# Kernel tuning notes

Measured on AMD Instinct MI355X. Metric: run time of the kernel, lower is better.

## Reference

```python
import jax, jax.numpy as jnp
import numpy as np

N_HEADS = 16
D_EMBED = 1024
HEAD_DIM = D_EMBED // N_HEADS


def setup_inputs() -> dict:
    key = jax.random.key(0)
    ks = jax.random.split(key, 9)
    s = 1.0 / np.sqrt(D_EMBED)
    def lin(kw, kb):
        W = jax.random.uniform(kw, (D_EMBED, D_EMBED), jnp.float32, -s, s)
        b = jax.random.uniform(kb, (D_EMBED,), jnp.float32, -s, s)
        return W, b
    q_w, q_b = lin(ks[0], ks[1])
    k_w, k_b = lin(ks[2], ks[3])
    v_w, v_b = lin(ks[4], ks[5])
    o_w, o_b = lin(ks[6], ks[7])
    x = jax.random.normal(ks[8], (4, 2048, D_EMBED), jnp.float32)
    return {"x": x, "q_w": q_w, "q_b": q_b, "k_w": k_w, "k_b": k_b,
            "v_w": v_w, "v_b": v_b, "o_w": o_w, "o_b": o_b}


def reference(x, q_w, q_b, k_w, k_b, v_w, v_b, o_w, o_b):
    B, S, _ = x.shape
    # projections; W stored as [in, out] so y = x @ W + b (matches nn.Linear math)
    def split_heads(y):
        return y.reshape(B, S, N_HEADS, HEAD_DIM).transpose(0, 2, 1, 3)  # [B,H,S,D]
    q = split_heads(x @ q_w + q_b)
    k = split_heads(x @ k_w + k_b)
    v = split_heads(x @ v_w + v_b)
    scale = 1.0 / np.sqrt(HEAD_DIM).astype(np.float32)
    scores = jnp.einsum('bhqd,bhkd->bhqk', q, k) * scale  # [B,H,S,S]
    weights = jax.nn.softmax(scores, axis=-1)
    attn = jnp.einsum('bhqk,bhkd->bhqd', weights, v)  # [B,H,S,D]
    attn = attn.transpose(0, 2, 1, 3).reshape(B, S, D_EMBED)
    return attn @ o_w + o_b
```

## Files before the change

### kernel.cpp

```cpp
#include <hip/hip_runtime.h>
#include <hip/hip_bf16.h>
#include <math.h>

typedef __attribute__((ext_vector_type(8))) short bf16x8;
typedef __attribute__((ext_vector_type(4))) float f32x4;

#define D_EMBED 1024
#define SEQ 2048
#define NH 16
#define HD 64
#define QSCALE 0.1803368801111204f

__device__ __forceinline__ short f2bf(float f) {
    union { float f; unsigned u; } v; v.f = f;
    return (short)((v.u + 0x7FFFu + ((v.u >> 16) & 1u)) >> 16);
}

__device__ __forceinline__ unsigned pk_bf16(float a, float b) {
#if __has_builtin(__builtin_amdgcn_cvt_pk_bf16_f32)
    typedef __attribute__((ext_vector_type(2))) __bf16 vbf2;
    union { vbf2 v; unsigned u; } c;
    c.v = __builtin_amdgcn_cvt_pk_bf16_f32(a, b);
    return c.u;
#else
    return (unsigned)(unsigned short)f2bf(a) | ((unsigned)(unsigned short)f2bf(b) << 16);
#endif
}

__device__ __forceinline__ float exp2f_(float x) {
#if __has_builtin(__builtin_amdgcn_exp2f)
    return __builtin_amdgcn_exp2f(x);
#else
    return __expf(x * 0.6931471805599453f);
#endif
}

typedef __attribute__((address_space(1))) const void gvoid_t;
typedef __attribute__((address_space(3))) void lvoid_t;
__device__ __forceinline__ void glds16(const void* g, void* l) {
    __builtin_amdgcn_global_load_lds((gvoid_t*)g, (lvoid_t*)l, 16, 0, 0);
}

__global__ __launch_bounds__(256) void xconv_kernel(const float* __restrict__ x,
                                                    short* __restrict__ xb)
{
    size_t i = ((size_t)blockIdx.x * 256 + threadIdx.x) * 8;
    float4 f0 = *(const float4*)(x + i);
    float4 f1 = *(const float4*)(x + i + 4);
    uint4 o;
    o.x = pk_bf16(f0.x, f0.y); o.y = pk_bf16(f0.z, f0.w);
    o.z = pk_bf16(f1.x, f1.y); o.w = pk_bf16(f1.z, f1.w);
    *(uint4*)(xb + i) = o;
}

__global__ __launch_bounds__(256) void wtrans_kernel(
    const float* __restrict__ w0, const float* __restrict__ w1,
    const float* __restrict__ w2, const float* __restrict__ w3,
    short* __restrict__ wt)
{
    __shared__ float tile[64][65];
    const float* W = (blockIdx.z == 0) ? w0 : (blockIdx.z == 1) ? w1
                   : (blockIdx.z == 2) ? w2 : w3;
    short* out = wt + (size_t)blockIdx.z * D_EMBED * D_EMBED;
    int k0 = blockIdx.x * 64, n0 = blockIdx.y * 64;
    #pragma unroll
    for (int i = 0; i < 16; i++) {
        int idx = threadIdx.x + i * 256; int r = idx >> 6, c = idx & 63;
        tile[r][c] = W[(size_t)(k0 + r) * D_EMBED + n0 + c];
    }
    __syncthreads();
    #pragma unroll
    for (int i = 0; i < 16; i++) {
        int idx = threadIdx.x + i * 256; int r = idx >> 6, c = idx & 63;
        out[(size_t)(n0 + r) * D_EMBED + k0 + c] = f2bf(tile[c][r]);
    }
}

__global__ __launch_bounds__(256) void gemm_qkv_kernel(
    const short* __restrict__ xb, const short* __restrict__ wt,
    const float* __restrict__ qb, const float* __restrict__ kb, const float* __restrict__ vb,
    short* __restrict__ qo, short* __restrict__ ko, short* __restrict__ vto)
{
    __shared__ __attribute__((aligned(16))) short As[128][32];
    __shared__ __attribute__((aligned(16))) short Bs[128][32];
    const int tid = threadIdx.x;
    const int lane = tid & 63, wv = tid >> 6;
    const int l16 = lane & 15, quad = lane >> 4;
    const int wm = (wv & 1) * 64, wn = (wv >> 1) * 64;
    const int m0 = blockIdx.y * 128, n0 = blockIdx.x * 128;

    const short* aptr0 = xb + (size_t)(m0 + (tid >> 2)) * D_EMBED + (tid & 3) * 8;
    const short* aptr1 = aptr0 + (size_t)64 * D_EMBED;
    const short* bptr0 = wt + (size_t)(n0 + (tid >> 2)) * D_EMBED + (tid & 3) * 8;
    const short* bptr1 = bptr0 + (size_t)64 * D_EMBED;
    char* aldsb = (char*)&As[0][0] + wv * 1024;
    char* bldsb = (char*)&Bs[0][0] + wv * 1024;

    f32x4 acc[4][4];
    #pragma unroll
    for (int a = 0; a < 4; a++)
        #pragma unroll
        for (int b = 0; b < 4; b++) acc[a][b] = (f32x4){0.f, 0.f, 0.f, 0.f};

    for (int k0 = 0; k0 < D_EMBED; k0 += 32) {
        __syncthreads();
        glds16(aptr0 + k0, aldsb);
        glds16(aptr1 + k0, aldsb + 4096);
        glds16(bptr0 + k0, bldsb);
        glds16(bptr1 + k0, bldsb + 4096);
        __syncthreads();
        bf16x8 af[4], bfr[4];
        #pragma unroll
        for (int mi = 0; mi < 4; mi++) af[mi]  = *(const bf16x8*)&As[wm + mi * 16 + l16][quad * 8];
        #pragma unroll
        for (int ni = 0; ni < 4; ni++) bfr[ni] = *(const bf16x8*)&Bs[wn + ni * 16 + l16][quad * 8];
        #pragma unroll
        for (int mi = 0; mi < 4; mi++)
            #pragma unroll
            for (int ni = 0; ni < 4; ni++)
                acc[mi][ni] = __builtin_amdgcn_mfma_f32_16x16x32_bf16(af[mi], bfr[ni], acc[mi][ni], 0, 0, 0);
    }

    const int zz = n0 >> 10;
    const int ncol0 = (n0 & 1023) + wn;
    const float* bias = (zz == 0) ? qb : (zz == 1) ? kb : vb;
    #pragma unroll
    for (int mi = 0; mi < 4; mi++)
        #pragma unroll
        for (int ni = 0; ni < 4; ni++)
            #pragma unroll
            for (int rg = 0; rg < 4; rg++) {
                int row = m0 + wm + mi * 16 + quad * 4 + rg;
                int col = ncol0 + ni * 16 + l16;
                float v = acc[mi][ni][rg] + bias[col];
                int b = row >> 11, s = row & 2047, h = col >> 6, d = col & 63;
                if (zz == 0)      qo[(((size_t)(b * NH + h)) * SEQ + s) * HD + d] = f2bf(v * QSCALE);
                else if (zz == 1) ko[(((size_t)(b * NH + h)) * SEQ + s) * HD + d] = f2bf(v);
                else              vto[(((size_t)(b * NH + h)) * HD + d) * SEQ + s] = f2bf(v);
            }
}

__global__ __launch_bounds__(256) void flash_kernel(
    const short* __restrict__ Q, const short* __restrict__ K,
    const short* __restrict__ Vt, short* __restrict__ attn)
{
    __shared__ __attribute__((aligned(16))) short Ks[64][64];
    __shared__ __attribute__((aligned(16))) short Vs[64][64];
    __shared__ __attribute__((aligned(16))) short Ps[4][64][72];
    const int bh = blockIdx.y, qt = blockIdx.x;
    const int tid = threadIdx.x, lane = tid & 63, wv = tid >> 6;
    const int l16 = lane & 15, quad = lane >> 4;
    const int sw = l16 & 7;

    bf16x8 qf[4][2];
    #pragma unroll
    for (int g = 0; g < 4; g++) {
        const short* qp = Q + ((size_t)bh * SEQ + qt * 256 + wv * 64 + g * 16 + l16) * HD;
        qf[g][0] = *(const bf16x8*)(qp + quad * 8);
        qf[g][1] = *(const bf16x8*)(qp + 32 + quad * 8);
    }

    const int sr = tid >> 3;
    const int scg = (tid & 7) ^ (sr & 7);
    const short* kp0 = K  + ((size_t)bh * SEQ + sr) * HD + scg * 8;
    const short* vp0 = Vt + ((size_t)bh * HD + sr) * SEQ + scg * 8;
    char* kldsb = (char*)&Ks[0][0] + wv * 1024;
    char* vldsb = (char*)&Vs[0][0] + wv * 1024;

    float lsum[4] = {0.f, 0.f, 0.f, 0.f};
    f32x4 oacc[4][4];
    #pragma unroll
    for (int g = 0; g < 4; g++)
        #pragma unroll
        for (int di = 0; di < 4; di++) oacc[g][di] = (f32x4){0.f, 0.f, 0.f, 0.f};

    for (int kt = 0; kt < SEQ; kt += 64) {
        __syncthreads();
        glds16(kp0 + (size_t)kt * HD, kldsb);
        glds16(kp0 + (size_t)(kt + 32) * HD, kldsb + 4096);
        glds16(vp0 + kt, vldsb);
        glds16(vp0 + (size_t)32 * SEQ + kt, vldsb + 4096);
        __syncthreads();

        bf16x8 kf[4][2];
        #pragma unroll
        for (int ni = 0; ni < 4; ni++) {
            kf[ni][0] = *(const bf16x8*)&Ks[ni * 16 + l16][((quad    ) ^ sw) * 8];
            kf[ni][1] = *(const bf16x8*)&Ks[ni * 16 + l16][((quad + 4) ^ sw) * 8];
        }

        #pragma unroll
        for (int g = 0; g < 4; g++) {
            f32x4 sacc[4];
            #pragma unroll
            for (int ni = 0; ni < 4; ni++) {
                sacc[ni] = (f32x4){0.f, 0.f, 0.f, 0.f};
                sacc[ni] = __builtin_amdgcn_mfma_f32_16x16x32_bf16(kf[ni][0], qf[g][0], sacc[ni], 0, 0, 0);
                sacc[ni] = __builtin_amdgcn_mfma_f32_16x16x32_bf16(kf[ni][1], qf[g][1], sacc[ni], 0, 0, 0);
            }
            short* prow = &Ps[wv][g * 16 + l16][0];
            float ps = 0.f;
            #pragma unroll
            for (int ni = 0; ni < 4; ni++) {
                float p0 = exp2f_(sacc[ni][0]);
                float p1 = exp2f_(sacc[ni][1]);
                float p2 = exp2f_(sacc[ni][2]);
                float p3 = exp2f_(sacc[ni][3]);
                ps += (p0 + p1) + (p2 + p3);
                uint2 pw; pw.x = pk_bf16(p0, p1); pw.y = pk_bf16(p2, p3);
                *(uint2*)(prow + ni * 16 + quad * 4) = pw;
            }
            lsum[g] += ps;
        }

        bf16x8 vf[4][2];
        #pragma unroll
        for (int di = 0; di < 4; di++) {
            vf[di][0] = *(const bf16x8*)&Vs[di * 16 + l16][((quad    ) ^ sw) * 8];
            vf[di][1] = *(const bf16x8*)&Vs[di * 16 + l16][((quad + 4) ^ sw) * 8];
        }
        #pragma unroll
        for (int g = 0; g < 4; g++) {
            const short* prow = &Ps[wv][g * 16 + l16][0];
            bf16x8 pf0 = *(const bf16x8*)(prow + quad * 8);
            bf16x8 pf1 = *(const bf16x8*)(prow + 32 + quad * 8);
            #pragma unroll
            for (int di = 0; di < 4; di++) {
                oacc[g][di] = __builtin_amdgcn_mfma_f32_16x16x32_bf16(pf0, vf[di][0], oacc[g][di], 0, 0, 0);
                oacc[g][di] = __builtin_amdgcn_mfma_f32_16x16x32_bf16(pf1, vf[di][1], oacc[g][di], 0, 0, 0);
            }
        }
    }

    const int b = bh >> 4, h = bh & 15;
    #pragma unroll
    for (int g = 0; g < 4; g++) {
        float l = lsum[g];
        l += __shfl_xor(l, 16);
        l += __shfl_xor(l, 32);
        float rl[4];
        #pragma unroll
        for (int rg = 0; rg < 4; rg++) rl[rg] = 1.0f / __shfl(l, quad * 4 + rg);
        #pragma unroll
        for (int di = 0; di < 4; di++)
            #pragma unroll
            for (int rg = 0; rg < 4; rg++) {
                int s = qt * 256 + wv * 64 + g * 16 + quad * 4 + rg;
                int col = h * HD + di * 16 + l16;
                attn[((size_t)b * SEQ + s) * D_EMBED + col] = f2bf(oacc[g][di][rg] * rl[rg]);
            }
    }
}

__global__ __launch_bounds__(256) void gemm_out_kernel(
    const short* __restrict__ attn, const short* __restrict__ wt_o,
    const float* __restrict__ ob, float* __restrict__ out)
{
    __shared__ __attribute__((aligned(16))) short As[128][32];
    __shared__ __attribute__((aligned(16))) short Bs[128][32];
    const int tid = threadIdx.x;
    const int lane = tid & 63, wv = tid >> 6;
    const int l16 = lane & 15, quad = lane >> 4;
    const int wm = (wv & 1) * 64, wn = (wv >> 1) * 64;
    const int m0 = blockIdx.y * 128, n0 = blockIdx.x * 128;

    const short* aptr0 = attn + (size_t)(m0 + (tid >> 2)) * D_EMBED + (tid & 3) * 8;
    const short* aptr1 = aptr0 + (size_t)64 * D_EMBED;
    const short* bptr0 = wt_o + (size_t)(n0 + (tid >> 2)) * D_EMBED + (tid & 3) * 8;
    const short* bptr1 = bptr0 + (size_t)64 * D_EMBED;
    char* aldsb = (char*)&As[0][0] + wv * 1024;
    char* bldsb = (char*)&Bs[0][0] + wv * 1024;

    f32x4 acc[4][4];
    #pragma unroll
    for (int a = 0; a < 4; a++)
        #pragma unroll
        for (int b = 0; b < 4; b++) acc[a][b] = (f32x4){0.f, 0.f, 0.f, 0.f};

    for (int k0 = 0; k0 < D_EMBED; k0 += 32) {
        __syncthreads();
        glds16(aptr0 + k0, aldsb);
        glds16(aptr1 + k0, aldsb + 4096);
        glds16(bptr0 + k0, bldsb);
        glds16(bptr1 + k0, bldsb + 4096);
        __syncthreads();
        bf16x8 af[4], bfr[4];
        #pragma unroll
        for (int mi = 0; mi < 4; mi++) af[mi]  = *(const bf16x8*)&As[wm + mi * 16 + l16][quad * 8];
        #pragma unroll
        for (int ni = 0; ni < 4; ni++) bfr[ni] = *(const bf16x8*)&Bs[wn + ni * 16 + l16][quad * 8];
        #pragma unroll
        for (int mi = 0; mi < 4; mi++)
            #pragma unroll
            for (int ni = 0; ni < 4; ni++)
                acc[mi][ni] = __builtin_amdgcn_mfma_f32_16x16x32_bf16(af[mi], bfr[ni], acc[mi][ni], 0, 0, 0);
    }

    #pragma unroll
    for (int mi = 0; mi < 4; mi++)
        #pragma unroll
        for (int ni = 0; ni < 4; ni++)
            #pragma unroll
            for (int rg = 0; rg < 4; rg++) {
                int row = m0 + wm + mi * 16 + quad * 4 + rg;
                int col = n0 + wn + ni * 16 + l16;
                out[(size_t)row * D_EMBED + col] = acc[mi][ni][rg] + ob[col];
            }
}

extern "C" void kernel_launch(void* const* d_in, const int* in_sizes, int n_in,
                              void* d_out, int out_size, void* d_ws, size_t ws_size,
                              hipStream_t stream) {
    const float* x  = (const float*)d_in[0];
    const float* qw = (const float*)d_in[1];
    const float* qb = (const float*)d_in[2];
    const float* kw = (const float*)d_in[3];
    const float* kb = (const float*)d_in[4];
    const float* vw = (const float*)d_in[5];
    const float* vb = (const float*)d_in[6];
    const float* ow = (const float*)d_in[7];
    const float* ob = (const float*)d_in[8];

    char* ws = (char*)d_ws;
    short* xb  = (short*)(ws);
    short* wt  = (short*)(ws + (size_t)(16 << 20));
    short* q   = (short*)(ws + (size_t)(24 << 20));
    short* k   = (short*)(ws + (size_t)(40 << 20));
    short* vt  = (short*)(ws + (size_t)(56 << 20));
    short* at  = xb;

    xconv_kernel<<<4096, 256, 0, stream>>>(x, xb);
    wtrans_kernel<<<dim3(16, 16, 4), 256, 0, stream>>>(qw, kw, vw, ow, wt);
    gemm_qkv_kernel<<<dim3(24, 64), 256, 0, stream>>>(xb, wt, qb, kb, vb, q, k, vt);
    flash_kernel<<<dim3(8, 64), 256, 0, stream>>>(q, k, vt, at);
    gemm_out_kernel<<<dim3(8, 64), 256, 0, stream>>>(at, wt + (size_t)3 * D_EMBED * D_EMBED, ob, (float*)d_out);
}
```

Before: 327.4 us.

## Split flash attention over two KV halves and stage V-transpose stores through LDS

The flash attention kernel gains a split-KV mode. Each block handles half of the key sequence and writes an unnormalized bf16 partial output plus its row sums. A new combine kernel then adds the two partials and normalizes them. The QKV GEMM epilogue for the V slice now stages the tile transposed in shared memory, so the transposed V output is written with coalesced 16-byte stores instead of scattered 2-byte writes. The split path only runs when the workspace is large enough. It costs an extra kernel launch and more global traffic for the partials, and storing the unnormalized partials in bf16 may lose precision.

After: 315.8 us. 3.5% less time.

```diff
diff --git a/kernel.cpp b/kernel.cpp
--- a/kernel.cpp
+++ b/kernel.cpp
@@ -83,6 +83,7 @@
 {
     __shared__ __attribute__((aligned(16))) short As[128][32];
     __shared__ __attribute__((aligned(16))) short Bs[128][32];
+    __shared__ __attribute__((aligned(16))) short Es[64][136];
     const int tid = threadIdx.x;
     const int lane = tid & 63, wv = tid >> 6;
     const int l16 = lane & 15, quad = lane >> 4;
@@ -122,32 +123,68 @@
     }
 
     const int zz = n0 >> 10;
-    const int ncol0 = (n0 & 1023) + wn;
-    const float* bias = (zz == 0) ? qb : (zz == 1) ? kb : vb;
-    #pragma unroll
-    for (int mi = 0; mi < 4; mi++)
-        #pragma unroll
-        for (int ni = 0; ni < 4; ni++)
-            #pragma unroll
-            for (int rg = 0; rg < 4; rg++) {
-                int row = m0 + wm + mi * 16 + quad * 4 + rg;
-                int col = ncol0 + ni * 16 + l16;
-                float v = acc[mi][ni][rg] + bias[col];
-                int b = row >> 11, s = row & 2047, h = col >> 6, d = col & 63;
-                if (zz == 0)      qo[(((size_t)(b * NH + h)) * SEQ + s) * HD + d] = f2bf(v * QSCALE);
-                else if (zz == 1) ko[(((size_t)(b * NH + h)) * SEQ + s) * HD + d] = f2bf(v);
-                else              vto[(((size_t)(b * NH + h)) * HD + d) * SEQ + s] = f2bf(v);
-            }
+    if (zz == 2) {
+        const int b = m0 >> 11, st0 = m0 & 2047;
+        const int hbase = (n0 & 1023) >> 6;
+        #pragma unroll
+        for (int h2 = 0; h2 < 2; h2++) {
+            __syncthreads();
+            if ((wv >> 1) == h2) {
+                #pragma unroll
+                for (int mi = 0; mi < 4; mi++) {
+                    int sbase = (wv & 1) * 64 + mi * 16 + quad * 4;
+                    #pragma unroll
+                    for (int ni = 0; ni < 4; ni++) {
+                        int d = ni * 16 + l16;
+                        float bv = vb[(n0 & 1023) + h2 * 64 + d];
+                        uint2 pw;
+                        pw.x = pk_bf16(acc[mi][ni][0] + bv, acc[mi][ni][1] + bv);
+                        pw.y = pk_bf16(acc[mi][ni][2] + bv, acc[mi][ni][3] + bv);
+                        *(uint2*)&Es[d][sbase] = pw;
+                    }
+                }
+            }
+            __syncthreads();
+            const int h = hbase + h2;
+            #pragma unroll
+            for (int j = 0; j < 4; j++) {
+                int d = j * 16 + (tid >> 4);
+                int sc = (tid & 15) * 8;
+                bf16x8 vv = *(const bf16x8*)&Es[d][sc];
+                *(bf16x8*)(vto + ((size_t)(b * NH + h) * HD + d) * SEQ + st0 + sc) = vv;
+            }
+        }
+    } else {
+        const int ncol0 = (n0 & 1023) + wn;
+        const float* bias = (zz == 0) ? qb : kb;
+        #pragma unroll
+        for (int mi = 0; mi < 4; mi++)
+            #pragma unroll
+            for (int ni = 0; ni < 4; ni++)
+                #pragma unroll
+                for (int rg = 0; rg < 4; rg++) {
+                    int row = m0 + wm + mi * 16 + quad * 4 + rg;
+                    int col = ncol0 + ni * 16 + l16;
+                    float v = acc[mi][ni][rg] + bias[col];
+                    int b = row >> 11, s = row & 2047, h = col >> 6, d = col & 63;
+                    if (zz == 0) qo[(((size_t)(b * NH + h)) * SEQ + s) * HD + d] = f2bf(v * QSCALE);
+                    else         ko[(((size_t)(b * NH + h)) * SEQ + s) * HD + d] = f2bf(v);
+                }
+    }
 }
 
 __global__ __launch_bounds__(256) void flash_kernel(
     const short* __restrict__ Q, const short* __restrict__ K,
-    const short* __restrict__ Vt, short* __restrict__ attn)
+    const short* __restrict__ Vt, short* __restrict__ attn,
+    short* __restrict__ Op0, short* __restrict__ Op1,
+    float* __restrict__ lp0, float* __restrict__ lp1,
+    int ktn, int mode)
 {
     __shared__ __attribute__((aligned(16))) short Ks[64][64];
     __shared__ __attribute__((aligned(16))) short Vs[64][64];
     __shared__ __attribute__((aligned(16))) short Ps[4][64][72];
     const int bh = blockIdx.y, qt = blockIdx.x;
+    const int kt0 = blockIdx.z * ktn;
     const int tid = threadIdx.x, lane = tid & 63, wv = tid >> 6;
     const int l16 = lane & 15, quad = lane >> 4;
     const int sw = l16 & 7;
@@ -174,7 +211,7 @@
         #pragma unroll
         for (int di = 0; di < 4; di++) oacc[g][di] = (f32x4){0.f, 0.f, 0.f, 0.f};
 
-    for (int kt = 0; kt < SEQ; kt += 64) {
+    for (int kt = kt0; kt < kt0 + ktn; kt += 64) {
         __syncthreads();
         glds16(kp0 + (size_t)kt * HD, kldsb);
         glds16(kp0 + (size_t)(kt + 32) * HD, kldsb + 4096);
@@ -233,23 +270,65 @@
     }
 
     const int b = bh >> 4, h = bh & 15;
+    short* Oz = blockIdx.z ? Op1 : Op0;
+    float* lz = blockIdx.z ? lp1 : lp0;
     #pragma unroll
     for (int g = 0; g < 4; g++) {
         float l = lsum[g];
         l += __shfl_xor(l, 16);
         l += __shfl_xor(l, 32);
-        float rl[4];
-        #pragma unroll
-        for (int rg = 0; rg < 4; rg++) rl[rg] = 1.0f / __shfl(l, quad * 4 + rg);
-        #pragma unroll
-        for (int di = 0; di < 4; di++)
-            #pragma unroll
-            for (int rg = 0; rg < 4; rg++) {
-                int s = qt * 256 + wv * 64 + g * 16 + quad * 4 + rg;
-                int col = h * HD + di * 16 + l16;
-                attn[((size_t)b * SEQ + s) * D_EMBED + col] = f2bf(oacc[g][di][rg] * rl[rg]);
-            }
-    }
+        if (mode) {
+            if (quad == 0) lz[(size_t)bh * SEQ + qt * 256 + wv * 64 + g * 16 + l16] = l;
+            #pragma unroll
+            for (int di = 0; di < 4; di++)
+                #pragma unroll
+                for (int rg = 0; rg < 4; rg++) {
+                    int s = qt * 256 + wv * 64 + g * 16 + quad * 4 + rg;
+                    int col = h * HD + di * 16 + l16;
+                    Oz[((size_t)b * SEQ + s) * D_EMBED + col] = f2bf(oacc[g][di][rg]);
+                }
+        } else {
+            float rl[4];
+            #pragma unroll
+            for (int rg = 0; rg < 4; rg++) rl[rg] = 1.0f / __shfl(l, quad * 4 + rg);
+            #pragma unroll
+            for (int di = 0; di < 4; di++)
+                #pragma unroll
+                for (int rg = 0; rg < 4; rg++) {
+                    int s = qt * 256 + wv * 64 + g * 16 + quad * 4 + rg;
+                    int col = h * HD + di * 16 + l16;
+                    attn[((size_t)b * SEQ + s) * D_EMBED + col] = f2bf(oacc[g][di][rg] * rl[rg]);
+                }
+        }
+    }
+}
+
+__global__ __launch_bounds__(256) void combine_kernel(
+    const short* __restrict__ Op0, const short* __restrict__ Op1,
+    const float* __restrict__ lp0, const float* __restrict__ lp1,
+    short* __restrict__ attn)
+{
+    size_t i = (size_t)blockIdx.x * 256 + threadIdx.x;
+    int r = (int)(i >> 7);
+    int c8 = ((int)i & 127) * 8;
+    int h = c8 >> 6, b = r >> 11, s = r & 2047;
+    float l = lp0[(size_t)(b * NH + h) * SEQ + s] + lp1[(size_t)(b * NH + h) * SEQ + s];
+    float rl = 1.0f / l;
+    uint4 a0 = *(const uint4*)(Op0 + i * 8);
+    uint4 a1 = *(const uint4*)(Op1 + i * 8);
+    uint4 o;
+    unsigned ua[4] = {a0.x, a0.y, a0.z, a0.w};
+    unsigned ub[4] = {a1.x, a1.y, a1.z, a1.w};
+    unsigned uo[4];
+    #pragma unroll
+    for (int j = 0; j < 4; j++) {
+        union { unsigned u; float f; } f0l, f0h, f1l, f1h;
+        f0l.u = (ua[j] & 0xffffu) << 16; f0h.u = ua[j] & 0xffff0000u;
+        f1l.u = (ub[j] & 0xffffu) << 16; f1h.u = ub[j] & 0xffff0000u;
+        uo[j] = pk_bf16((f0l.f + f1l.f) * rl, (f0h.f + f1h.f) * rl);
+    }
+    o.x = uo[0]; o.y = uo[1]; o.z = uo[2]; o.w = uo[3];
+    *(uint4*)(attn + i * 8) = o;
 }
 
 __global__ __launch_bounds__(256) void gemm_out_kernel(
@@ -329,9 +408,22 @@
     short* vt  = (short*)(ws + (size_t)(56 << 20));
     short* at  = xb;
 
+    const bool split = ws_size >= (size_t)105 * 1024 * 1024;
+    short* Op0 = (short*)(ws + (size_t)(72 << 20));
+    short* Op1 = (short*)(ws + (size_t)(88 << 20));
+    float* lp0 = (float*)(ws + (size_t)(104 << 20));
+    float* lp1 = (float*)(ws + (size_t)(104 << 20) + SEQ * 64 * sizeof(float));
+
     xconv_kernel<<<4096, 256, 0, stream>>>(x, xb);
     wtrans_kernel<<<dim3(16, 16, 4), 256, 0, stream>>>(qw, kw, vw, ow, wt);
     gemm_qkv_kernel<<<dim3(24, 64), 256, 0, stream>>>(xb, wt, qb, kb, vb, q, k, vt);
-    flash_kernel<<<dim3(8, 64), 256, 0, stream>>>(q, k, vt, at);
+    if (split) {
+        flash_kernel<<<dim3(8, 64, 2), 256, 0, stream>>>(q, k, vt, at, Op0, Op1, lp0, lp1,
+                                                         SEQ / 2, 1);
+        combine_kernel<<<(8192 * 1024 / 8) / 256, 256, 0, stream>>>(Op0, Op1, lp0, lp1, at);
+    } else {
+        flash_kernel<<<dim3(8, 64, 1), 256, 0, stream>>>(q, k, vt, at, at, at, lp0, lp0,
+                                                         SEQ, 0);
+    }
     gemm_out_kernel<<<dim3(8, 64), 256, 0, stream>>>(at, wt + (size_t)3 * D_EMBED * D_EMBED, ob, (float*)d_out);
 }
```
